# Kernel tuning notes

Hardware: AMD Instinct MI355X
Metric: run time of the kernel (lower is better)

Reference implementation:

```python
import jax, jax.numpy as jnp
import numpy as np


def lstm_encode(x, Wih, Whh, b):
    """x: [S, T, F] -> final hidden state [S, H]. PyTorch LSTM gate order (i, f, g, o)."""
    S = x.shape[0]
    H = Whh.shape[1]

    def step(carry, xt):
        h, c = carry
        z = xt @ Wih.T + h @ Whh.T + b  # [S, 4H]
        i, f, g, o = jnp.split(z, 4, axis=-1)
        c = jax.nn.sigmoid(f) * c + jax.nn.sigmoid(i) * jnp.tanh(g)
        h = jax.nn.sigmoid(o) * jnp.tanh(c)
        return (h, c), None

    init = (jnp.zeros((S, H), x.dtype), jnp.zeros((S, H), x.dtype))
    (h, _), _ = jax.lax.scan(step, init, jnp.swapaxes(x, 0, 1))
    return h


def gatv2(h, Ws, Wd, a, bias):
    """Dense GATv2 on batched fully-connected graphs (no self loops).
    h: [G, N, Hin]; Ws, Wd: [nh, Hin, O]; a: [nh, O]; bias: [nh, O] -> [G, N, nh, O].
    Graph is fully connected (all i != j), so edge-softmax == dense row softmax
    with the diagonal masked out; this is the efficient dense form of the
    gather / LeakyReLU / edge-softmax / scatter pattern in DGL's GATv2Conv."""
    nh = Ws.shape[0]
    N = h.shape[1]
    self_mask = jnp.eye(N, dtype=bool)
    outs = []
    for hd in range(nh):  # small fixed head count; loop caps peak memory
        fs = h @ Ws[hd]  # [G, N, O] source-projected feats (messages)
        fd = h @ Wd[hd]  # [G, N, O] dst-projected feats
        e = jax.nn.leaky_relu(fd[:, :, None, :] + fs[:, None, :, :], 0.2)  # [G, dst, src, O]
        logits = jnp.where(self_mask, -jnp.inf, e @ a[hd])  # [G, dst, src]
        attn = jax.nn.softmax(logits, axis=-1)
        outs.append(jnp.einsum('gds,gso->gdo', attn, fs) + bias[hd])
    return jnp.stack(outs, axis=2)


def cosine(x, y, eps=1e-6):
    xn = x / jnp.maximum(jnp.linalg.norm(x, axis=-1, keepdims=True), eps)
    yn = y / jnp.maximum(jnp.linalg.norm(y, axis=-1, keepdims=True), eps)
    return (xn * yn).sum(-1)


def setup_inputs() -> dict:
    key = jax.random.key(0)
    B, K, T, N, F, H, GH, NH = 16, 4, 64, 128, 16, 32, 32, 8
    ks = jax.random.split(key, 16)

    def rn(k, shape, scale=1.0):
        return jax.random.normal(k, shape, jnp.float32) * scale

    return {
        'anchor': rn(ks[0], (B, T, N, F)),
        'pos': rn(ks[1], (B, T, N, F)),
        'neg': rn(ks[2], (B, K, T, N, F)),
        'hideout': rn(ks[3], (B, 2)),
        'timestep': jax.random.uniform(ks[4], (B, 1), jnp.float32),
        'Wih': rn(ks[5], (4 * H, F), 1.0 / np.sqrt(F)),
        'Whh': rn(ks[6], (4 * H, H), 1.0 / np.sqrt(H)),
        'b_lstm': rn(ks[7], (4 * H,), 0.1),
        'W1s': rn(ks[8], (NH, H, H), 1.0 / np.sqrt(H)),
        'W1d': rn(ks[9], (NH, H, H), 1.0 / np.sqrt(H)),
        'a1': rn(ks[10], (NH, H), 1.0 / np.sqrt(H)),
        'b1': rn(ks[11], (NH, H), 0.1),
        'W2s': rn(ks[12], (1, H, GH), 1.0 / np.sqrt(H)),
        'W2d': rn(ks[13], (1, H, GH), 1.0 / np.sqrt(H)),
        'a2': rn(ks[14], (1, GH), 1.0 / np.sqrt(GH)),
        'b2': rn(ks[15], (1, GH), 0.1),
        'num_agents': 128,
    }


def reference(anchor, pos, neg, hideout, timestep, Wih, Whh, b_lstm,
              W1s, W1d, a1, b1, W2s, W2d, a2, b2, num_agents):
    B, T, N, F = anchor.shape
    K = neg.shape[1]
    H = Whh.shape[1]
    # per-agent time series -> LSTM sequences
    a_seq = jnp.transpose(anchor, (0, 2, 1, 3)).reshape(B * N, T, F)
    p_seq = jnp.transpose(pos, (0, 2, 1, 3)).reshape(B * N, T, F)
    n_seq = jnp.transpose(neg, (0, 1, 3, 2, 4)).reshape(B * K * N, T, F)
    hn = lstm_encode(jnp.concatenate([a_seq, p_seq, n_seq], 0), Wih, Whh, b_lstm)
    hg = hn.reshape(-1, N, H)  # [(2+K)*B, N, H] batched fully-connected graphs
    h1 = gatv2(hg, W1s, W1d, a1, b1).mean(axis=2)  # mean over 8 heads
    h2 = gatv2(h1, W2s, W2d, a2, b2)[:, :, 0, :]   # single head, squeezed
    pooled = h2.mean(axis=1)                        # AvgPooling over nodes
    anchor_res = pooled[:B]
    pos_res = pooled[B:2 * B]
    neg_res = pooled[2 * B:].reshape(B, K, -1)
    sim_pos = cosine(anchor_res, pos_res)[:, None]      # [B, 1]
    sim_neg = cosine(anchor_res[:, None, :], neg_res)   # [B, K]
    all_vecs = jnp.concatenate([sim_neg, sim_pos], axis=1)  # positive last
    contrastive = (-jax.nn.log_softmax(all_vecs, axis=1)[:, -1]).mean()
    res = jnp.concatenate([anchor_res, hideout, timestep], axis=-1)
    return res, contrastive
```

## Files before the change

kernel.cpp:

```cpp
#include <hip/hip_runtime.h>
#include <math.h>


typedef __bf16 bf16x8 __attribute__((ext_vector_type(8)));
typedef float  f32x4  __attribute__((ext_vector_type(4)));
typedef unsigned int u32x4 __attribute__((ext_vector_type(4)));

__device__ __forceinline__ float fast_rcp(float x) { return __builtin_amdgcn_rcpf(x); }
__device__ __forceinline__ float sigm(float x)     { return fast_rcp(1.f + __expf(-x)); }
__device__ __forceinline__ float tanh_fast(float x){ return fmaf(2.f, fast_rcp(1.f + __expf(-2.f * x)), -1.f); }

#define KEEP4(x) asm volatile("" : "+v"(x))

__global__ __launch_bounds__(512, 1) void lstm_mfma_kernel(
    const float* __restrict__ anchor, const float* __restrict__ pos,
    const float* __restrict__ neg, const float* __restrict__ Wih,
    const float* __restrict__ Whh, const float* __restrict__ bias,
    float* __restrict__ hn)
{
    __shared__ float Zl[8 * 592];
    __shared__ unsigned int Hbuf[2][512];
    const int tid  = threadIdx.x;
    const int w    = tid >> 6;
    const int lane = tid & 63;
    const int l15  = lane & 15;
    const int g4   = lane >> 4;
    const int am   = tid >> 5;
    const int aj   = tid & 31;

    #pragma unroll
    for (int i = 0; i < 2; ++i) ((unsigned int*)Hbuf)[tid + i * 512] = 0u;

    const int G = w >> 1, Hh = w & 1;
    const int c = G * 32 + Hh * 16 + l15;
    u32x4 whhH, whhL, wihH;
    {
        union { u32x4 u; bf16x8 v; } th, tl, ti;
        const float* wr = Whh + c * 32 + g4 * 8;
        #pragma unroll
        for (int i = 0; i < 8; ++i) {
            float wv = wr[i];
            __bf16 hi = (__bf16)wv;
            th.v[i] = hi;
            tl.v[i] = (__bf16)(wv - (float)hi);
        }
        if (g4 < 2) {
            const float* wr2 = Wih + c * 16 + g4 * 8;
            #pragma unroll
            for (int i = 0; i < 8; ++i) ti.v[i] = (__bf16)wr2[i];
        } else {
            #pragma unroll
            for (int i = 0; i < 8; ++i) ti.v[i] = (__bf16)0.f;
        }
        whhH = th.u; whhL = tl.u; wihH = ti.u;
    }
    KEEP4(whhH); KEEP4(whhL); KEEP4(wihH);

    const float bi = bias[aj], bf_ = bias[32 + aj], bg = bias[64 + aj], bo = bias[96 + aj];

    const int s = blockIdx.x * 16 + l15;
    const float* xbase; int sl;
    if (s < 2048)      { xbase = anchor; sl = s; }
    else if (s < 4096) { xbase = pos;    sl = s - 2048; }
    else               { xbase = neg;    sl = s - 4096; }
    const bool xact = (g4 < 2);
    const float* xp = xbase + (sl >> 7) * 131072 + (sl & 127) * 16 + (xact ? g4 * 8 : 0);

    const float4 z4 = make_float4(0.f, 0.f, 0.f, 0.f);
    float4 xaA = z4, xbA = z4, xaB = z4, xbB = z4;
    if (xact) {
        xaA = *(const float4*)(xp);        xbA = *(const float4*)(xp + 4);
        xaB = *(const float4*)(xp + 2048); xbB = *(const float4*)(xp + 2052);
    }

    float cstA = 0.f, hA = 0.f;

    const int c0  = g4 * 2;
    const int swz = l15 & 7;
    const int ro0 = l15 * 32 + ((c0 ^ swz) << 2);
    const int ro1 = l15 * 32 + (((c0 + 1) ^ swz) << 2);
    const int zw  = w * 592 + (g4 * 4) * 36 + l15;
    const int tHh = aj >> 4, jc = am * 36 + (aj & 15);
    const int zr_i = (0 | tHh) * 592 + jc;
    const int zr_f = (2 | tHh) * 592 + jc;
    const int zr_g = (4 | tHh) * 592 + jc;
    const int zr_o = (6 | tHh) * 592 + jc;
    const int hw   = am * 32 + (((aj >> 2) ^ (am & 7)) << 2) + (aj & 3);
    int cur = 0;
    __syncthreads();

    #define LSTM_STEP(XA, XB)                                                          \
    {                                                                                  \
        bf16x8 ax;                                                                     \
        ax[0]=(__bf16)XA.x; ax[1]=(__bf16)XA.y; ax[2]=(__bf16)XA.z; ax[3]=(__bf16)XA.w;\
        ax[4]=(__bf16)XB.x; ax[5]=(__bf16)XB.y; ax[6]=(__bf16)XB.z; ax[7]=(__bf16)XB.w;\
        uint4 v0 = *(const uint4*)(Hbuf[cur] + ro0);                                   \
        uint4 v1 = *(const uint4*)(Hbuf[cur] + ro1);                                   \
        union { unsigned int u[4]; bf16x8 v; } ahi;                                    \
        ahi.u[0] = __builtin_amdgcn_perm(v0.y, v0.x, 0x05040100u);                     \
        ahi.u[1] = __builtin_amdgcn_perm(v0.w, v0.z, 0x05040100u);                     \
        ahi.u[2] = __builtin_amdgcn_perm(v1.y, v1.x, 0x05040100u);                     \
        ahi.u[3] = __builtin_amdgcn_perm(v1.w, v1.z, 0x05040100u);                     \
        f32x4 a = __builtin_amdgcn_mfma_f32_16x16x32_bf16(                             \
            ax, __builtin_bit_cast(bf16x8, wihH), (f32x4)(0.f), 0, 0, 0);              \
        a = __builtin_amdgcn_mfma_f32_16x16x32_bf16(                                   \
            ahi.v, __builtin_bit_cast(bf16x8, whhH), a, 0, 0, 0);                      \
        a = __builtin_amdgcn_mfma_f32_16x16x32_bf16(                                   \
            ahi.v, __builtin_bit_cast(bf16x8, whhL), a, 0, 0, 0);                      \
        Zl[zw]       = a[0];                                                           \
        Zl[zw + 36]  = a[1];                                                           \
        Zl[zw + 72]  = a[2];                                                           \
        Zl[zw + 108] = a[3];                                                           \
        __syncthreads();                                                               \
        float zi = Zl[zr_i] + bi;                                                      \
        float zf = Zl[zr_f] + bf_;                                                     \
        float zg = Zl[zr_g] + bg;                                                      \
        float zo = Zl[zr_o] + bo;                                                      \
        float cn = fmaf(sigm(zf), cstA, sigm(zi) * tanh_fast(zg));                     \
        cstA = cn;                                                                     \
        hA = sigm(zo) * tanh_fast(cn);                                                 \
        Hbuf[cur ^ 1][hw] = (unsigned int)__builtin_bit_cast(unsigned short,           \
                                                             (__bf16)hA);             \
        __syncthreads();                                                               \
        cur ^= 1;                                                                      \
    }

    for (int t = 0; t < 64; t += 2) {
        float4 cA1 = xaA, cA2 = xbA;
        if (xact && t + 2 < 64) {
            const float* p = xp + (t + 2) * 2048;
            xaA = *(const float4*)(p); xbA = *(const float4*)(p + 4);
        }
        LSTM_STEP(cA1, cA2);

        float4 cB1 = xaB, cB2 = xbB;
        if (xact && t + 3 < 64) {
            const float* p = xp + (t + 3) * 2048;
            xaB = *(const float4*)(p); xbB = *(const float4*)(p + 4);
        }
        LSTM_STEP(cB1, cB2);
    }
    #undef LSTM_STEP

    hn[(blockIdx.x * 16 + am) * 32 + aj] = hA;
}

__device__ __forceinline__ int fsoff(int n) { return n * 36 + ((n >> 5) << 2); }

__global__ __launch_bounds__(256, 2) void gat1_kernel(
    const float* __restrict__ hn, const float* __restrict__ W1s,
    const float* __restrict__ W1d, const float* __restrict__ a1,
    const float* __restrict__ b1, float* __restrict__ h1heads)
{
    const int g = blockIdx.x >> 3, hd = blockIdx.x & 7;
    __shared__ float FSf[128 * 36 + 16];
    __shared__ float FD[128][36];
    __shared__ float AVr[32];
    __shared__ float As06[128];
    __shared__ float Ad06[128];
    const int tid = threadIdx.x;

    if (tid < 32) AVr[tid] = a1[hd * 32 + tid];

    {
        const int wv = tid >> 6, lane = tid & 63;
        const int l15 = lane & 15, g4 = lane >> 4;
        const int colbase = (wv & 1) * 16;
        const bool isFD = (wv >> 1) != 0;
        const float* Wmat = isFD ? W1d : W1s;

        u32x4 bH, bL;
        {
            union { u32x4 u; bf16x8 v; } th, tl;
            const float* wp = Wmat + hd * 1024 + (g4 * 8) * 32 + colbase + l15;
            #pragma unroll
            for (int i = 0; i < 8; ++i) {
                float wvv = wp[i * 32];
                __bf16 hi = (__bf16)wvv;
                th.v[i] = hi;
                tl.v[i] = (__bf16)(wvv - (float)hi);
            }
            bH = th.u; bL = tl.u;
        }

        #pragma unroll 1
        for (int t = 0; t < 8; ++t) {
            const float* hp = hn + (size_t)(g * 128 + t * 16 + l15) * 32 + g4 * 8;
            float4 a0 = *(const float4*)(hp);
            float4 a1v = *(const float4*)(hp + 4);
            union { u32x4 u; bf16x8 v; } axh, axl;
            axh.v[0]=(__bf16)a0.x;  axl.v[0]=(__bf16)(a0.x-(float)axh.v[0]);
            axh.v[1]=(__bf16)a0.y;  axl.v[1]=(__bf16)(a0.y-(float)axh.v[1]);
            axh.v[2]=(__bf16)a0.z;  axl.v[2]=(__bf16)(a0.z-(float)axh.v[2]);
            axh.v[3]=(__bf16)a0.w;  axl.v[3]=(__bf16)(a0.w-(float)axh.v[3]);
            axh.v[4]=(__bf16)a1v.x; axl.v[4]=(__bf16)(a1v.x-(float)axh.v[4]);
            axh.v[5]=(__bf16)a1v.y; axl.v[5]=(__bf16)(a1v.y-(float)axh.v[5]);
            axh.v[6]=(__bf16)a1v.z; axl.v[6]=(__bf16)(a1v.z-(float)axh.v[6]);
            axh.v[7]=(__bf16)a1v.w; axl.v[7]=(__bf16)(a1v.w-(float)axh.v[7]);

            f32x4 cc = __builtin_amdgcn_mfma_f32_16x16x32_bf16(
                axh.v, __builtin_bit_cast(bf16x8, bH), (f32x4)(0.f), 0, 0, 0);
            cc = __builtin_amdgcn_mfma_f32_16x16x32_bf16(
                axl.v, __builtin_bit_cast(bf16x8, bH), cc, 0, 0, 0);
            cc = __builtin_amdgcn_mfma_f32_16x16x32_bf16(
                axh.v, __builtin_bit_cast(bf16x8, bL), cc, 0, 0, 0);

            const int r0 = t * 16 + g4 * 4;
            const int col = colbase + l15;
            if (!isFD) {
                FSf[fsoff(r0 + 0) + col] = cc[0];
                FSf[fsoff(r0 + 1) + col] = cc[1];
                FSf[fsoff(r0 + 2) + col] = cc[2];
                FSf[fsoff(r0 + 3) + col] = cc[3];
            } else {
                FD[r0 + 0][col] = cc[0];
                FD[r0 + 1][col] = cc[1];
                FD[r0 + 2][col] = cc[2];
                FD[r0 + 3][col] = cc[3];
            }
        }
    }
    __syncthreads();

    if (tid < 128) {
        float ss = 0.f, sd = 0.f;
        const float* fr = FSf + fsoff(tid);
        #pragma unroll
        for (int oo = 0; oo < 32; ++oo) {
            int o = (oo + tid) & 31;
            float a = AVr[o];
            ss = fmaf(a, fr[o], ss);
            sd = fmaf(a, FD[tid][o], sd);
        }
        As06[tid] = 0.6f * ss;
        Ad06[tid] = 0.6f * sd;
    }
    __syncthreads();

    const int p = tid >> 2, sq = tid & 3, sbase = sq << 5;
    const int d0 = p, d1 = p + 64;
    float fdr0[32], fdr1[32], avs[32];
    #pragma unroll
    for (int c = 0; c < 8; ++c) {
        float4 v0 = *(const float4*)&FD[d0][c * 4];
        fdr0[c*4+0] = v0.x; fdr0[c*4+1] = v0.y; fdr0[c*4+2] = v0.z; fdr0[c*4+3] = v0.w;
        float4 v1 = *(const float4*)&FD[d1][c * 4];
        fdr1[c*4+0] = v1.x; fdr1[c*4+1] = v1.y; fdr1[c*4+2] = v1.z; fdr1[c*4+3] = v1.w;
        float4 wv = *(const float4*)&AVr[c * 4];
        avs[c*4+0] = 0.4f * wv.x; avs[c*4+1] = 0.4f * wv.y;
        avs[c*4+2] = 0.4f * wv.z; avs[c*4+3] = 0.4f * wv.w;
    }
    const float adc0 = Ad06[d0], adc1 = Ad06[d1];

    float Z0 = 0.f, Z1 = 0.f;
    float acc0[32], acc1[32];
    #pragma unroll
    for (int o = 0; o < 32; ++o) { acc0[o] = 0.f; acc1[o] = 0.f; }
    #pragma unroll 1
    for (int si = 0; si < 32; ++si) {
        const int s = sbase + si;
        const float* fr = FSf + fsoff(s);
        float4 fa[8];
        #pragma unroll
        for (int c = 0; c < 8; ++c) fa[c] = *(const float4*)(fr + c * 4);
        float c00 = 0.f, c01 = 0.f, c02 = 0.f, c03 = 0.f;
        float c10 = 0.f, c11 = 0.f, c12 = 0.f, c13 = 0.f;
        #pragma unroll
        for (int c = 0; c < 8; ++c) {
            float e;
            e = fdr0[c*4+0] + fa[c].x; c00 = fmaf(avs[c*4+0], __builtin_fabsf(e), c00);
            e = fdr1[c*4+0] + fa[c].x; c10 = fmaf(avs[c*4+0], __builtin_fabsf(e), c10);
            e = fdr0[c*4+1] + fa[c].y; c01 = fmaf(avs[c*4+1], __builtin_fabsf(e), c01);
            e = fdr1[c*4+1] + fa[c].y; c11 = fmaf(avs[c*4+1], __builtin_fabsf(e), c11);
            e = fdr0[c*4+2] + fa[c].z; c02 = fmaf(avs[c*4+2], __builtin_fabsf(e), c02);
            e = fdr1[c*4+2] + fa[c].z; c12 = fmaf(avs[c*4+2], __builtin_fabsf(e), c12);
            e = fdr0[c*4+3] + fa[c].w; c03 = fmaf(avs[c*4+3], __builtin_fabsf(e), c03);
            e = fdr1[c*4+3] + fa[c].w; c13 = fmaf(avs[c*4+3], __builtin_fabsf(e), c13);
        }
        const float ass = As06[s];
        float v0 = adc0 + ass + ((c00 + c01) + (c02 + c03));
        float v1 = adc1 + ass + ((c10 + c11) + (c12 + c13));
        float e0 = (s == d0) ? 0.f : __expf(v0);
        float e1 = (s == d1) ? 0.f : __expf(v1);
        Z0 += e0; Z1 += e1;
        #pragma unroll
        for (int c = 0; c < 8; ++c) {
            acc0[c*4+0] = fmaf(e0, fa[c].x, acc0[c*4+0]);
            acc1[c*4+0] = fmaf(e1, fa[c].x, acc1[c*4+0]);
            acc0[c*4+1] = fmaf(e0, fa[c].y, acc0[c*4+1]);
            acc1[c*4+1] = fmaf(e1, fa[c].y, acc1[c*4+1]);
            acc0[c*4+2] = fmaf(e0, fa[c].z, acc0[c*4+2]);
            acc1[c*4+2] = fmaf(e1, fa[c].z, acc1[c*4+2]);
            acc0[c*4+3] = fmaf(e0, fa[c].w, acc0[c*4+3]);
            acc1[c*4+3] = fmaf(e1, fa[c].w, acc1[c*4+3]);
        }
    }
    Z0 += __shfl_xor(Z0, 1); Z0 += __shfl_xor(Z0, 2);
    Z1 += __shfl_xor(Z1, 1); Z1 += __shfl_xor(Z1, 2);
    const float rz0 = fast_rcp(Z0), rz1 = fast_rcp(Z1);
    #pragma unroll
    for (int o = 0; o < 32; ++o) {
        acc0[o] += __shfl_xor(acc0[o], 1);
        acc0[o] += __shfl_xor(acc0[o], 2);
        acc1[o] += __shfl_xor(acc1[o], 1);
        acc1[o] += __shfl_xor(acc1[o], 2);
    }

    if (sq == 0) {
        const float* bp = b1 + hd * 32;
        float* dst0 = h1heads + ((size_t)((g * 8 + hd) * 128 + d0)) * 32;
        float* dst1 = h1heads + ((size_t)((g * 8 + hd) * 128 + d1)) * 32;
        #pragma unroll
        for (int c = 0; c < 8; ++c) {
            float4 v;
            v.x = fmaf(acc0[c*4+0], rz0, bp[c*4+0]);
            v.y = fmaf(acc0[c*4+1], rz0, bp[c*4+1]);
            v.z = fmaf(acc0[c*4+2], rz0, bp[c*4+2]);
            v.w = fmaf(acc0[c*4+3], rz0, bp[c*4+3]);
            *(float4*)(dst0 + c * 4) = v;
            v.x = fmaf(acc1[c*4+0], rz1, bp[c*4+0]);
            v.y = fmaf(acc1[c*4+1], rz1, bp[c*4+1]);
            v.z = fmaf(acc1[c*4+2], rz1, bp[c*4+2]);
            v.w = fmaf(acc1[c*4+3], rz1, bp[c*4+3]);
            *(float4*)(dst1 + c * 4) = v;
        }
    }
}

__global__ __launch_bounds__(256) void gat2_kernel(
    const float* __restrict__ h1heads, const float* __restrict__ W2s,
    const float* __restrict__ W2d, const float* __restrict__ a2,
    const float* __restrict__ b2, float* __restrict__ pooled)
{
    const int g = blockIdx.x;
    __shared__ float HS[128][36];
    __shared__ float FSf[128 * 36 + 16];
    __shared__ float FD[128][36];
    __shared__ float AVr[32];
    __shared__ float As06[128];
    __shared__ float Ad06[128];
    const int tid = threadIdx.x;

    if (tid < 32) AVr[tid] = a2[tid];

    {
        #pragma unroll
        for (int i = 0; i < 4; ++i) {
            int idx4 = i * 256 + tid;
            float sx = 0.f, sy = 0.f, sz = 0.f, sw = 0.f;
            #pragma unroll
            for (int hdd = 0; hdd < 8; ++hdd) {
                const float4* src = (const float4*)(h1heads + (size_t)(g * 8 + hdd) * 4096);
                float4 v = src[idx4];
                sx += v.x; sy += v.y; sz += v.z; sw += v.w;
            }
            int n = idx4 >> 3, k0 = (idx4 & 7) * 4;
            float4 r; r.x = sx * 0.125f; r.y = sy * 0.125f; r.z = sz * 0.125f; r.w = sw * 0.125f;
            *(float4*)&HS[n][k0] = r;
        }
    }
    __syncthreads();

    {
        const int o = tid & 31, nb = tid >> 5;
        float wcs[32], wcd[32];
        const float* wsp = W2s + o;
        const float* wdp = W2d + o;
        #pragma unroll
        for (int k = 0; k < 32; ++k) { wcs[k] = wsp[k * 32]; wcd[k] = wdp[k * 32]; }
        #pragma unroll 1
        for (int n = nb * 16; n < nb * 16 + 16; ++n) {
            float a0 = 0.f, a1_ = 0.f, b0 = 0.f, b1_ = 0.f;
            #pragma unroll
            for (int k0 = 0; k0 < 32; k0 += 4) {
                const float4 hv = *(const float4*)&HS[n][k0];
                a0 = fmaf(hv.x, wcs[k0+0], a0); b0 = fmaf(hv.x, wcd[k0+0], b0);
                a1_ = fmaf(hv.y, wcs[k0+1], a1_); b1_ = fmaf(hv.y, wcd[k0+1], b1_);
                a0 = fmaf(hv.z, wcs[k0+2], a0); b0 = fmaf(hv.z, wcd[k0+2], b0);
                a1_ = fmaf(hv.w, wcs[k0+3], a1_); b1_ = fmaf(hv.w, wcd[k0+3], b1_);
            }
            FSf[fsoff(n) + o] = a0 + a1_;
            FD[n][o] = b0 + b1_;
        }
    }
    __syncthreads();

    if (tid < 128) {
        float ss = 0.f, sd = 0.f;
        const float* fr = FSf + fsoff(tid);
        #pragma unroll
        for (int oo = 0; oo < 32; ++oo) {
            int o = (oo + tid) & 31;
            float a = AVr[o];
            ss = fmaf(a, fr[o], ss);
            sd = fmaf(a, FD[tid][o], sd);
        }
        As06[tid] = 0.6f * ss;
        Ad06[tid] = 0.6f * sd;
    }
    __syncthreads();

    const int d = tid >> 1, sbase = (tid & 1) << 6;
    float fdr[32], avs[32];
    #pragma unroll
    for (int c = 0; c < 8; ++c) {
        float4 v = *(const float4*)&FD[d][c * 4];
        fdr[c*4+0] = v.x; fdr[c*4+1] = v.y; fdr[c*4+2] = v.z; fdr[c*4+3] = v.w;
        float4 wv = *(const float4*)&AVr[c * 4];
        avs[c*4+0] = 0.4f * wv.x; avs[c*4+1] = 0.4f * wv.y;
        avs[c*4+2] = 0.4f * wv.z; avs[c*4+3] = 0.4f * wv.w;
    }
    const float adc = Ad06[d];

    float Z = 0.f;
    float acc[32];
    #pragma unroll
    for (int o = 0; o < 32; ++o) acc[o] = 0.f;
    #pragma unroll 1
    for (int si = 0; si < 64; ++si) {
        const int s = sbase + si;
        const float* fr = FSf + fsoff(s);
        float4 fa[8];
        #pragma unroll
        for (int c = 0; c < 8; ++c) fa[c] = *(const float4*)(fr + c * 4);
        float c0 = 0.f, c1 = 0.f, c2 = 0.f, c3 = 0.f;
        #pragma unroll
        for (int c = 0; c < 8; ++c) {
            float e0 = fdr[c*4+0] + fa[c].x; c0 = fmaf(avs[c*4+0], __builtin_fabsf(e0), c0);
            float e1 = fdr[c*4+1] + fa[c].y; c1 = fmaf(avs[c*4+1], __builtin_fabsf(e1), c1);
            float e2 = fdr[c*4+2] + fa[c].z; c2 = fmaf(avs[c*4+2], __builtin_fabsf(e2), c2);
            float e3 = fdr[c*4+3] + fa[c].w; c3 = fmaf(avs[c*4+3], __builtin_fabsf(e3), c3);
        }
        float v = adc + As06[s] + ((c0 + c1) + (c2 + c3));
        float e = (s == d) ? 0.f : __expf(v);
        Z += e;
        #pragma unroll
        for (int c = 0; c < 8; ++c) {
            acc[c*4+0] = fmaf(e, fa[c].x, acc[c*4+0]);
            acc[c*4+1] = fmaf(e, fa[c].y, acc[c*4+1]);
            acc[c*4+2] = fmaf(e, fa[c].z, acc[c*4+2]);
            acc[c*4+3] = fmaf(e, fa[c].w, acc[c*4+3]);
        }
    }
    Z += __shfl_xor(Z, 1);
    const float rz = fast_rcp(Z);
    #pragma unroll
    for (int o = 0; o < 32; ++o) acc[o] += __shfl_xor(acc[o], 1);

    __syncthreads();
    if ((tid & 1) == 0) {
        #pragma unroll
        for (int c = 0; c < 4; ++c) {
            float4 v;
            v.x = acc[c*4+0] * rz; v.y = acc[c*4+1] * rz;
            v.z = acc[c*4+2] * rz; v.w = acc[c*4+3] * rz;
            *(float4*)&FD[d][c * 4] = v;
        }
    } else {
        #pragma unroll
        for (int c = 4; c < 8; ++c) {
            float4 v;
            v.x = acc[c*4+0] * rz; v.y = acc[c*4+1] * rz;
            v.z = acc[c*4+2] * rz; v.w = acc[c*4+3] * rz;
            *(float4*)&FD[d][c * 4] = v;
        }
    }
    __syncthreads();

    if (tid < 32) {
        float sp = 0.f;
        #pragma unroll 1
        for (int n = 0; n < 128; ++n) sp += FD[n][tid];
        pooled[g * 32 + tid] = fmaf(sp, 1.f / 128.f, b2[tid]);
    }
}

__global__ void final_kernel(const float* __restrict__ pooled,
                             const float* __restrict__ hideout,
                             const float* __restrict__ timestep,
                             float* __restrict__ out)
{
    const int b = threadIdx.x;
    __shared__ float lossArr[16];
    if (b < 16) {
        const float* A  = pooled + b * 32;
        const float* Pv = pooled + (16 + b) * 32;
        float av[32];
        float na = 0.f;
        #pragma unroll
        for (int i = 0; i < 32; ++i) { av[i] = A[i]; na += av[i] * av[i]; }
        float npv = 0.f, dp = 0.f;
        #pragma unroll
        for (int i = 0; i < 32; ++i) { float p = Pv[i]; npv += p * p; dp += av[i] * p; }
        const float eps = 1e-6f;
        const float ia = 1.f / fmaxf(sqrtf(na), eps);
        const float sp = dp * ia / fmaxf(sqrtf(npv), eps);
        float sn[4];
        #pragma unroll
        for (int k = 0; k < 4; ++k) {
            const float* Nv = pooled + (32 + b * 4 + k) * 32;
            float nn = 0.f, dn = 0.f;
            #pragma unroll
            for (int i = 0; i < 32; ++i) { float q = Nv[i]; nn += q * q; dn += av[i] * q; }
            sn[k] = dn * ia / fmaxf(sqrtf(nn), eps);
        }
        float m = sp;
        #pragma unroll
        for (int k = 0; k < 4; ++k) m = fmaxf(m, sn[k]);
        float Z = expf(sp - m);
        #pragma unroll
        for (int k = 0; k < 4; ++k) Z += expf(sn[k] - m);
        lossArr[b] = logf(Z) + m - sp;
        float* r = out + b * 35;
        #pragma unroll
        for (int i = 0; i < 32; ++i) r[i] = av[i];
        r[32] = hideout[b * 2];
        r[33] = hideout[b * 2 + 1];
        r[34] = timestep[b];
    }
    __syncthreads();
    if (b == 0) {
        float s = 0.f;
        #pragma unroll
        for (int i = 0; i < 16; ++i) s += lossArr[i];
        out[560] = s * (1.f / 16.f);
    }
}

extern "C" void kernel_launch(void* const* d_in, const int* in_sizes, int n_in,
                              void* d_out, int out_size, void* d_ws, size_t ws_size,
                              hipStream_t stream) {
    const float* anchor   = (const float*)d_in[0];
    const float* pos      = (const float*)d_in[1];
    const float* neg      = (const float*)d_in[2];
    const float* hideout  = (const float*)d_in[3];
    const float* timestep = (const float*)d_in[4];
    const float* Wih      = (const float*)d_in[5];
    const float* Whh      = (const float*)d_in[6];
    const float* b_lstm   = (const float*)d_in[7];
    const float* W1s      = (const float*)d_in[8];
    const float* W1d      = (const float*)d_in[9];
    const float* a1       = (const float*)d_in[10];
    const float* b1       = (const float*)d_in[11];
    const float* W2s      = (const float*)d_in[12];
    const float* W2d      = (const float*)d_in[13];
    const float* a2       = (const float*)d_in[14];
    const float* b2       = (const float*)d_in[15];
    float* out = (float*)d_out;

    char* ws = (char*)d_ws;
    float* hn      = (float*)(ws);
    float* h1heads = (float*)(ws + 1605632);
    float* pooled  = (float*)(ws + 14188544);

    hipLaunchKernelGGL(lstm_mfma_kernel, dim3(768), dim3(512), 0, stream,
                       anchor, pos, neg, Wih, Whh, b_lstm, hn);
    hipLaunchKernelGGL(gat1_kernel,  dim3(768),  dim3(256), 0, stream,
                       hn, W1s, W1d, a1, b1, h1heads);
    hipLaunchKernelGGL(gat2_kernel,  dim3(96),   dim3(256), 0, stream,
                       h1heads, W2s, W2d, a2, b2, pooled);
    hipLaunchKernelGGL(final_kernel, dim3(1),    dim3(64),  0, stream,
                       pooled, hideout, timestep, out);
}
```

Before: 147.3 us.

## Regroup LSTM gate columns per wave and exchange via shuffles instead of LDS

Weight rows are permuted so that each wave's MFMA output holds all four gates for the hidden units it owns. The gate values are then redistributed within the wave with cross-lane shuffles, which removes the LDS staging buffer and one block-wide barrier per time step. This trades the LDS round trip and barrier for 16 shuffles per step plus selects, on a latency-bound recurrent loop.

```diff
diff --git a/kernel.cpp b/kernel.cpp
--- a/kernel.cpp
+++ b/kernel.cpp
@@ -18,25 +18,21 @@
     const float* __restrict__ Whh, const float* __restrict__ bias,
     float* __restrict__ hn)
 {
-    __shared__ float Zl[8 * 592];
     __shared__ unsigned int Hbuf[2][512];
     const int tid  = threadIdx.x;
     const int w    = tid >> 6;
     const int lane = tid & 63;
     const int l15  = lane & 15;
     const int g4   = lane >> 4;
-    const int am   = tid >> 5;
-    const int aj   = tid & 31;
 
     #pragma unroll
     for (int i = 0; i < 2; ++i) ((unsigned int*)Hbuf)[tid + i * 512] = 0u;
 
-    const int G = w >> 1, Hh = w & 1;
-    const int c = G * 32 + Hh * 16 + l15;
+    const int wrow = (l15 >> 2) * 32 + 4 * w + (l15 & 3);
     u32x4 whhH, whhL, wihH;
     {
         union { u32x4 u; bf16x8 v; } th, tl, ti;
-        const float* wr = Whh + c * 32 + g4 * 8;
+        const float* wr = Whh + wrow * 32 + g4 * 8;
         #pragma unroll
         for (int i = 0; i < 8; ++i) {
             float wv = wr[i];
@@ -45,7 +41,7 @@
             tl.v[i] = (__bf16)(wv - (float)hi);
         }
         if (g4 < 2) {
-            const float* wr2 = Wih + c * 16 + g4 * 8;
+            const float* wr2 = Wih + wrow * 16 + g4 * 8;
             #pragma unroll
             for (int i = 0; i < 8; ++i) ti.v[i] = (__bf16)wr2[i];
         } else {
@@ -56,7 +52,10 @@
     }
     KEEP4(whhH); KEEP4(whhL); KEEP4(wihH);
 
-    const float bi = bias[aj], bf_ = bias[32 + aj], bg = bias[64 + aj], bo = bias[96 + aj];
+    const int aseq  = lane >> 2;
+    const int aunit = 4 * w + (lane & 3);
+    const float bi = bias[aunit],       bf_ = bias[32 + aunit];
+    const float bg = bias[64 + aunit],  bo  = bias[96 + aunit];
 
     const int s = blockIdx.x * 16 + l15;
     const float* xbase; int sl;
@@ -79,13 +78,9 @@
     const int swz = l15 & 7;
     const int ro0 = l15 * 32 + ((c0 ^ swz) << 2);
     const int ro1 = l15 * 32 + (((c0 + 1) ^ swz) << 2);
-    const int zw  = w * 592 + (g4 * 4) * 36 + l15;
-    const int tHh = aj >> 4, jc = am * 36 + (aj & 15);
-    const int zr_i = (0 | tHh) * 592 + jc;
-    const int zr_f = (2 | tHh) * 592 + jc;
-    const int zr_g = (4 | tHh) * 592 + jc;
-    const int zr_o = (6 | tHh) * 592 + jc;
-    const int hw   = am * 32 + (((aj >> 2) ^ (am & 7)) << 2) + (aj & 3);
+    const int hw  = aseq * 32 + (((aunit >> 2) ^ (aseq & 7)) << 2) + (aunit & 3);
+    const int sbase = (lane & 0x30) + (lane & 3);
+    const int myr   = (lane >> 2) & 3;
     int cur = 0;
     __syncthreads();
 
@@ -107,16 +102,19 @@
             ahi.v, __builtin_bit_cast(bf16x8, whhH), a, 0, 0, 0);                      \
         a = __builtin_amdgcn_mfma_f32_16x16x32_bf16(                                   \
             ahi.v, __builtin_bit_cast(bf16x8, whhL), a, 0, 0, 0);                      \
-        Zl[zw]       = a[0];                                                           \
-        Zl[zw + 36]  = a[1];                                                           \
-        Zl[zw + 72]  = a[2];                                                           \
-        Zl[zw + 108] = a[3];                                                           \
-        __syncthreads();                                                               \
-        float zi = Zl[zr_i] + bi;                                                      \
-        float zf = Zl[zr_f] + bf_;                                                     \
-        float zg = Zl[zr_g] + bg;                                                      \
-        float zo = Zl[zr_o] + bo;                                                      \
-        float cn = fmaf(sigm(zf), cstA, sigm(zi) * tanh_fast(zg));                     \
+                \
+                \
+        float zi = 0.f, zf = 0.f, zg_ = 0.f, zo = 0.f;                                 \
+        _Pragma("unroll")                                                              \
+        for (int r = 0; r < 4; ++r) {                                                  \
+            float t0 = __shfl(a[r], sbase);                                            \
+            float t1 = __shfl(a[r], sbase + 4);                                        \
+            float t2 = __shfl(a[r], sbase + 8);                                        \
+            float t3 = __shfl(a[r], sbase + 12);                                       \
+            if (myr == r) { zi = t0; zf = t1; zg_ = t2; zo = t3; }                     \
+        }                                                                              \
+        zi += bi; zf += bf_; zg_ += bg; zo += bo;                                      \
+        float cn = fmaf(sigm(zf), cstA, sigm(zi) * tanh_fast(zg_));                    \
         cstA = cn;                                                                     \
         hA = sigm(zo) * tanh_fast(cn);                                                 \
         Hbuf[cur ^ 1][hw] = (unsigned int)__builtin_bit_cast(unsigned short,           \
@@ -142,7 +140,7 @@
     }
     #undef LSTM_STEP
 
-    hn[(blockIdx.x * 16 + am) * 32 + aj] = hA;
+    hn[(blockIdx.x * 16 + aseq) * 32 + aunit] = hA;
 }
 
 __device__ __forceinline__ int fsoff(int n) { return n * 36 + ((n >> 5) << 2); }
```

Result: slower. 177.5 us (+20.5%).
